# Kernel tuning notes

Measured on AMD Instinct MI355X. Metric: run time of the kernel, lower is better.

The kernel has to match this reference:

```python
import jax, jax.numpy as jnp
import numpy as np

N_NODES = 15000
N_EDGES = 400000
H_DIM = 128
N_RELS = 237
N_BASES = 100


def rel_graph_conv(x, src, dst, etype, norm, V, comp, loop_w, bias, n_nodes):
    """DGL RelGraphConv with basis regularizer, self_loop=True, bias=True.

    W_r = sum_b comp[r, b] * V[b]; message m_e = (x[src_e] @ W_{etype_e}) * norm_e;
    h[v] = sum_{e: dst_e = v} m_e + x[v] @ loop_w + bias.
    Reordered as sum over bases to avoid materializing per-edge weights:
      h = sum_b segment_sum(coef[etype, b] * norm * x[src], dst) @ V[b]
    """
    x_src = x[src] * norm                      # [E, D] (norm is [E, 1])
    coef = comp[etype]                         # [E, B]
    d_out = V.shape[2]

    def body(acc, cv):
        c, Vb = cv                             # c: [E], Vb: [D, Dout]
        agg = jax.ops.segment_sum(x_src * c[:, None], dst, num_segments=n_nodes)
        return acc + agg @ Vb, None

    init = jnp.zeros((n_nodes, d_out), x.dtype)
    h, _ = jax.lax.scan(body, init, (coef.T, V))  # scan over B bases
    return h + bias + x @ loop_w


def setup_inputs() -> dict:
    key = jax.random.key(0)
    ks = jax.random.split(key, 16)
    s = 1.0 / np.sqrt(H_DIM)
    inp = {
        "nids": jnp.arange(N_NODES, dtype=jnp.int32),
        "src": jax.random.randint(ks[0], (N_EDGES,), 0, N_NODES),
        "dst": jax.random.randint(ks[1], (N_EDGES,), 0, N_NODES),
        "etype": jax.random.randint(ks[2], (N_EDGES,), 0, N_RELS),
        "norm": jax.random.uniform(ks[3], (N_EDGES, 1), dtype=jnp.float32),
        "edge_weights": jax.random.normal(ks[4], (N_EDGES,), dtype=jnp.float32),
        "emb": jax.random.normal(ks[5], (N_NODES, H_DIM), dtype=jnp.float32) * s,
        "V1": jax.random.normal(ks[6], (N_BASES, H_DIM, H_DIM), dtype=jnp.float32) * s,
        "comp1": jax.random.normal(ks[7], (N_RELS, N_BASES), dtype=jnp.float32) * (1.0 / np.sqrt(N_BASES)),
        "loop1": jax.random.normal(ks[8], (H_DIM, H_DIM), dtype=jnp.float32) * s,
        "bias1": jnp.zeros((H_DIM,), dtype=jnp.float32),
        "V2": jax.random.normal(ks[9], (N_BASES, H_DIM, H_DIM), dtype=jnp.float32) * s,
        "comp2": jax.random.normal(ks[10], (N_RELS, N_BASES), dtype=jnp.float32) * (1.0 / np.sqrt(N_BASES)),
        "loop2": jax.random.normal(ks[11], (H_DIM, H_DIM), dtype=jnp.float32) * s,
        "bias2": jnp.zeros((H_DIM,), dtype=jnp.float32),
    }
    return inp


def reference(nids, src, dst, etype, norm, edge_weights, emb, V1, comp1, loop1, bias1, V2, comp2, loop2, bias2):
    # edge_weights is accepted but unused by the original forward.
    x = emb[nids]                                              # embedding lookup
    n = x.shape[0]
    h = jax.nn.relu(rel_graph_conv(x, src, dst, etype, norm, V1, comp1, loop1, bias1, n))
    # dropout(p=0.2) treated as identity (eval mode)
    h = rel_graph_conv(h, src, dst, etype, norm, V2, comp2, loop2, bias2, n)
    return h
```

## Files before the change

### kernel.cpp

```cpp
#include <hip/hip_runtime.h>
#include <hip/hip_bf16.h>


typedef unsigned short u16;
typedef unsigned int   u32;
typedef __bf16 bf16x8 __attribute__((ext_vector_type(8)));
typedef float  f32x4  __attribute__((ext_vector_type(4)));
typedef u32    u32x2  __attribute__((ext_vector_type(2)));

#define N_NODES 15000
#define N_EDGES 400000
#define N_RELS  237
#define N_BASES 100
#define NT_MAX  1800
#define NB_SORT 196
#define CHUNK   2048

__device__ __forceinline__ u32 packbf(float a, float b) {
    u16 lo = __builtin_bit_cast(u16, (__bf16)a);
    u16 hi = __builtin_bit_cast(u16, (__bf16)b);
    return (u32)lo | ((u32)hi << 16);
}
__device__ __forceinline__ float bfbits2f(u32 hi16) {
    u32 x = hi16 << 16;
    return __builtin_bit_cast(float, x);
}

__global__ __launch_bounds__(256) void histA_kernel(const int* __restrict__ etype,
                                                    int* __restrict__ blockHist) {
    __shared__ int hh[256];
    int tid = threadIdx.x, b = blockIdx.x;
    hh[tid] = 0;
    __syncthreads();
    int e0 = b * CHUNK;
    int e1 = e0 + CHUNK; if (e1 > N_EDGES) e1 = N_EDGES;
    for (int e = e0 + tid; e < e1; e += 256)
        atomicAdd(&hh[etype[e]], 1);
    __syncthreads();
    if (tid < N_RELS) blockHist[tid * NB_SORT + b] = hh[tid];
}

__global__ __launch_bounds__(256) void scanB_kernel(const int* __restrict__ blockHist,
                                                    int* __restrict__ baseOff,
                                                    int2* __restrict__ tiles,
                                                    int* __restrict__ tileCount) {
    __shared__ int h[256], o[256], to[256];
    int tid = threadIdx.x;
    int sum = 0;
    if (tid < N_RELS)
        for (int b = 0; b < NB_SORT; ++b) sum += blockHist[tid * NB_SORT + b];
    h[tid] = (tid < N_RELS) ? sum : 0;
    __syncthreads();
    if (tid == 0) {
        int run = 0, tc = 0;
        for (int r = 0; r < N_RELS; ++r) {
            o[r] = run; run += h[r];
            to[r] = tc; tc += (h[r] + 255) >> 8;
        }
        *tileCount = tc;
    }
    __syncthreads();
    if (tid < N_RELS) {
        int n = h[tid], t0 = to[tid], base = o[tid];
        for (int t = 0; t * 256 < n; ++t) {
            int nE = n - t * 256; if (nE > 256) nE = 256;
            tiles[t0 + t] = make_int2(base + t * 256, (tid << 9) | nE);
        }
        int run = base;
        for (int b = 0; b < NB_SORT; ++b) {
            baseOff[tid * NB_SORT + b] = run;
            run += blockHist[tid * NB_SORT + b];
        }
    }
}

__global__ __launch_bounds__(256) void scatterC_kernel(const int* __restrict__ etype,
                                                       const int* __restrict__ src,
                                                       const float* __restrict__ norm,
                                                       const int* __restrict__ baseOff,
                                                       int* __restrict__ perm,
                                                       int* __restrict__ srcPerm,
                                                       float* __restrict__ normPerm) {
    __shared__ int lcur[256];
    int tid = threadIdx.x, b = blockIdx.x;
    if (tid < N_RELS) lcur[tid] = baseOff[tid * NB_SORT + b];
    __syncthreads();
    int e0 = b * CHUNK;
    int e1 = e0 + CHUNK; if (e1 > N_EDGES) e1 = N_EDGES;
    for (int e = e0 + tid; e < e1; e += 256) {
        int r = etype[e];
        int pos = atomicAdd(&lcur[r], 1);
        perm[pos] = e;
        srcPerm[pos] = src[e];
        normPerm[pos] = norm[e];
    }
}

__global__ __launch_bounds__(256) void zeroDeg_kernel(int* __restrict__ deg) {
    int i = blockIdx.x * 256 + threadIdx.x;
    if (i < N_NODES) deg[i] = 0;
}
__global__ __launch_bounds__(256) void degcnt_kernel(const int* __restrict__ dst,
                                                     int* __restrict__ deg) {
    for (int e = blockIdx.x * 256 + threadIdx.x; e < N_EDGES; e += gridDim.x * 256)
        atomicAdd(&deg[dst[e]], 1);
}
__global__ __launch_bounds__(256) void scanDeg_kernel(const int* __restrict__ deg,
                                                      int* __restrict__ rowptr,
                                                      int* __restrict__ cursor) {
    __shared__ int part[256];
    int tid = threadIdx.x;
    const int R = 59;
    int lo = tid * R, hi = lo + R; if (hi > N_NODES + 1) hi = N_NODES + 1;
    int s = 0;
    for (int i = lo; i < hi; ++i) s += (i < N_NODES) ? deg[i] : 0;
    part[tid] = s;
    __syncthreads();
    if (tid == 0) {
        int run = 0;
        for (int t = 0; t < 256; ++t) { int tmp = part[t]; part[t] = run; run += tmp; }
    }
    __syncthreads();
    int run = part[tid];
    for (int i = lo; i < hi; ++i) {
        rowptr[i] = run; cursor[i] = run;
        run += (i < N_NODES) ? deg[i] : 0;
    }
}
__global__ __launch_bounds__(256) void scatterDst_kernel(const int* __restrict__ dst,
                                                         const int* __restrict__ perm,
                                                         int* __restrict__ cursor,
                                                         int* __restrict__ dstSlots) {
    for (int s = blockIdx.x * 256 + threadIdx.x; s < N_EDGES; s += gridDim.x * 256) {
        int e = perm[s];
        int v = dst[e];
        int pos = atomicAdd(&cursor[v], 1);
        dstSlots[pos] = s;
    }
}

__global__ __launch_bounds__(256) void wgemm_kernel(const float* __restrict__ comp,
                                                    const float* __restrict__ V,
                                                    u16* __restrict__ outRM) {
    __shared__ float cls[128 * 33];
    __shared__ float vls[32 * 256];
    int tid = threadIdx.x;
    int r0 = blockIdx.x * 32, n0 = blockIdx.y * 256;
    for (int idx = tid; idx < 32 * 128; idx += 256) {
        int rr = idx >> 7, b = idx & 127;
        float v = 0.f;
        if (b < N_BASES && (r0 + rr) < N_RELS) v = comp[(size_t)(r0 + rr) * N_BASES + b];
        cls[b * 33 + rr] = v;
    }
    float acc[4][8];
    #pragma unroll
    for (int i = 0; i < 4; ++i)
        #pragma unroll
        for (int j = 0; j < 8; ++j) acc[i][j] = 0.f;
    int rgrp = tid >> 5, ngrp = tid & 31;
    for (int bc = 0; bc < 4; ++bc) {
        __syncthreads();
        for (int idx = tid; idx < 32 * 256; idx += 256) {
            int bb = idx >> 8, n = idx & 255;
            int b = bc * 32 + bb;
            vls[idx] = (b < N_BASES) ? V[(size_t)b * 16384 + n0 + n] : 0.f;
        }
        __syncthreads();
        #pragma unroll 4
        for (int bb = 0; bb < 32; ++bb) {
            float a_[4];
            #pragma unroll
            for (int i = 0; i < 4; ++i) a_[i] = cls[(bc * 32 + bb) * 33 + rgrp * 4 + i];
            float4 b0 = *(const float4*)&vls[bb * 256 + ngrp * 8];
            float4 b1 = *(const float4*)&vls[bb * 256 + ngrp * 8 + 4];
            #pragma unroll
            for (int i = 0; i < 4; ++i) {
                acc[i][0] += a_[i] * b0.x; acc[i][1] += a_[i] * b0.y;
                acc[i][2] += a_[i] * b0.z; acc[i][3] += a_[i] * b0.w;
                acc[i][4] += a_[i] * b1.x; acc[i][5] += a_[i] * b1.y;
                acc[i][6] += a_[i] * b1.z; acc[i][7] += a_[i] * b1.w;
            }
        }
    }
    #pragma unroll
    for (int i = 0; i < 4; ++i) {
        int r = r0 + rgrp * 4 + i;
        if (r < N_RELS) {
            bf16x8 pk;
            #pragma unroll
            for (int j = 0; j < 8; ++j) pk[j] = (__bf16)acc[i][j];
            *(bf16x8*)(outRM + (size_t)r * 16384 + n0 + ngrp * 8) = pk;
        }
    }
}

__global__ __launch_bounds__(256) void transp_kernel(const u16* __restrict__ in,
                                                     u16* __restrict__ outT) {
    __shared__ u16 tls[128 * 130];
    int r = blockIdx.x, tid = threadIdx.x;
    const u32* inu = (const u32*)(in + (size_t)r * 16384);
    #pragma unroll
    for (int i = 0; i < 32; ++i) {
        int idx = i * 256 + tid;
        u32 v = inu[idx];
        int k = idx >> 6, jp = idx & 63;
        tls[k * 130 + jp * 2]     = (u16)(v & 0xffffu);
        tls[k * 130 + jp * 2 + 1] = (u16)(v >> 16);
    }
    __syncthreads();
    u32* outu = (u32*)(outT + (size_t)r * 16384);
    #pragma unroll
    for (int i = 0; i < 32; ++i) {
        int idx = i * 256 + tid;
        int col = idx >> 6, kk2 = idx & 63;
        u32 v = (u32)tls[(2 * kk2) * 130 + col] | ((u32)tls[(2 * kk2 + 1) * 130 + col] << 16);
        outu[col * 64 + kk2] = v;
    }
}

__global__ __launch_bounds__(256) void loopT_kernel(const float* __restrict__ lw,
                                                    u16* __restrict__ outT) {
    int tid = threadIdx.x;
    u32* outu = (u32*)outT;
    #pragma unroll
    for (int i = 0; i < 32; ++i) {
        int idx = i * 256 + tid;
        int col = idx >> 6, kk2 = idx & 63;
        float a = lw[(size_t)(2 * kk2) * 128 + col];
        float b = lw[(size_t)(2 * kk2 + 1) * 128 + col];
        outu[col * 64 + kk2] = packbf(a, b);
    }
}

__global__ __launch_bounds__(256) void xbf_kernel(const float* __restrict__ x,
                                                  u16* __restrict__ xbf,
                                                  int reluIn) {
    int i = blockIdx.x * 256 + threadIdx.x;
    if (i >= N_NODES * 16) return;
    const float4* xp = (const float4*)x;
    float4 f0 = xp[i * 2], f1 = xp[i * 2 + 1];
    if (reluIn) {
        f0.x = fmaxf(f0.x, 0.f); f0.y = fmaxf(f0.y, 0.f);
        f0.z = fmaxf(f0.z, 0.f); f0.w = fmaxf(f0.w, 0.f);
        f1.x = fmaxf(f1.x, 0.f); f1.y = fmaxf(f1.y, 0.f);
        f1.z = fmaxf(f1.z, 0.f); f1.w = fmaxf(f1.w, 0.f);
    }
    uint4 pk;
    pk.x = packbf(f0.x, f0.y); pk.y = packbf(f0.z, f0.w);
    pk.z = packbf(f1.x, f1.y); pk.w = packbf(f1.z, f1.w);
    ((uint4*)xbf)[i] = pk;
}

__global__ __launch_bounds__(256) void init_mfma_kernel(const float* __restrict__ xin,
                                                        const u16* __restrict__ lwT,
                                                        const float* __restrict__ bias,
                                                        float* __restrict__ hout,
                                                        int reluIn) {
    __shared__ u16 xlds[8192];
    int v0 = blockIdx.x * 64;
    int tid = threadIdx.x, lane = tid & 63, w = tid >> 6;

    bf16x8 bfr[2][4];
    #pragma unroll
    for (int n2 = 0; n2 < 2; ++n2) {
        int col = w * 32 + n2 * 16 + (lane & 15);
        #pragma unroll
        for (int ks = 0; ks < 4; ++ks) {
            int k0 = ks * 32 + (lane >> 4) * 8;
            bfr[n2][ks] = *(const bf16x8*)(lwT + (size_t)col * 128 + k0);
        }
    }

    {
        int s = tid >> 2, p = tid & 3;
        int row = v0 + s;
        if (row < N_NODES) {
            const float4* xr = (const float4*)(xin + (size_t)row * 128 + p * 32);
            #pragma unroll
            for (int c = 0; c < 4; ++c) {
                float4 f0 = xr[c * 2], f1 = xr[c * 2 + 1];
                if (reluIn) {
                    f0.x = fmaxf(f0.x, 0.f); f0.y = fmaxf(f0.y, 0.f);
                    f0.z = fmaxf(f0.z, 0.f); f0.w = fmaxf(f0.w, 0.f);
                    f1.x = fmaxf(f1.x, 0.f); f1.y = fmaxf(f1.y, 0.f);
                    f1.z = fmaxf(f1.z, 0.f); f1.w = fmaxf(f1.w, 0.f);
                }
                bf16x8 pk;
                pk[0] = (__bf16)f0.x; pk[1] = (__bf16)f0.y;
                pk[2] = (__bf16)f0.z; pk[3] = (__bf16)f0.w;
                pk[4] = (__bf16)f1.x; pk[5] = (__bf16)f1.y;
                pk[6] = (__bf16)f1.z; pk[7] = (__bf16)f1.w;
                int ch = p * 4 + c;
                *(bf16x8*)((char*)xlds + s * 256 + ((ch * 16) ^ ((s & 7) << 4))) = pk;
            }
        } else {
            bf16x8 z = {(__bf16)0.f, (__bf16)0.f, (__bf16)0.f, (__bf16)0.f,
                        (__bf16)0.f, (__bf16)0.f, (__bf16)0.f, (__bf16)0.f};
            #pragma unroll
            for (int c = 0; c < 4; ++c) {
                int ch = p * 4 + c;
                *(bf16x8*)((char*)xlds + s * 256 + ((ch * 16) ^ ((s & 7) << 4))) = z;
            }
        }
    }
    __syncthreads();

    #pragma unroll
    for (int rt = 0; rt < 4; ++rt) {
        bf16x8 af[4];
        int arow = rt * 16 + (lane & 15);
        #pragma unroll
        for (int ks = 0; ks < 4; ++ks) {
            int k0 = ks * 32 + (lane >> 4) * 8;
            af[ks] = *(const bf16x8*)((const char*)xlds + arow * 256 + ((k0 * 2) ^ ((arow & 7) << 4)));
        }
        f32x4 acc[2];
        acc[0] = (f32x4){0.f, 0.f, 0.f, 0.f};
        acc[1] = (f32x4){0.f, 0.f, 0.f, 0.f};
        #pragma unroll
        for (int ks = 0; ks < 4; ++ks) {
            acc[0] = __builtin_amdgcn_mfma_f32_16x16x32_bf16(bfr[0][ks], af[ks], acc[0], 0, 0, 0);
            acc[1] = __builtin_amdgcn_mfma_f32_16x16x32_bf16(bfr[1][ks], af[ks], acc[1], 0, 0, 0);
        }
        int orow = v0 + rt * 16 + (lane & 15);
        if (orow < N_NODES) {
            #pragma unroll
            for (int n2 = 0; n2 < 2; ++n2) {
                int fbase = w * 32 + n2 * 16 + ((lane >> 4) << 2);
                float4 bv = *(const float4*)(bias + fbase);
                float4 o;
                o.x = acc[n2][0] + bv.x; o.y = acc[n2][1] + bv.y;
                o.z = acc[n2][2] + bv.z; o.w = acc[n2][3] + bv.w;
                *(float4*)(hout + (size_t)orow * 128 + fbase) = o;
            }
        }
    }
}

__global__ __launch_bounds__(256) void msg_kernel(const u16* __restrict__ xbf,
                                                  const int* __restrict__ srcPerm,
                                                  const int2* __restrict__ tiles,
                                                  const int* __restrict__ tileCount,
                                                  const u16* __restrict__ WbtT,
                                                  u16* __restrict__ msg) {
    __shared__ u16 xlds[8192];
    int bid = blockIdx.x;
    int tile = (bid & 7) * (NT_MAX / 8) + (bid >> 3);
    if (tile >= *tileCount) return;
    int2 td = tiles[tile];
    int slot0 = td.x;
    int r  = td.y >> 9;
    int nE = td.y & 511;
    int tid = threadIdx.x, lane = tid & 63, w = tid >> 6;

    bf16x8 bfr[2][4];
    #pragma unroll
    for (int n2 = 0; n2 < 2; ++n2) {
        int col = w * 32 + n2 * 16 + (lane & 15);
        #pragma unroll
        for (int ks = 0; ks < 4; ++ks) {
            int k0 = ks * 32 + (lane >> 4) * 8;
            bfr[n2][ks] = *(const bf16x8*)(WbtT + (size_t)r * 16384 + col * 128 + k0);
        }
    }

    for (int s0 = 0; s0 < nE; s0 += 64) {
        int cnt = nE - s0; if (cnt > 64) cnt = 64;
        __syncthreads();
        {
            int s = tid >> 2, p = tid & 3;
            if (s < cnt) {
                int xrow = srcPerm[slot0 + s0 + s];
                const uint4* xr = (const uint4*)(xbf + (size_t)xrow * 128);
                #pragma unroll
                for (int c = 0; c < 4; ++c) {
                    int ch = p * 4 + c;
                    *(uint4*)((char*)xlds + s * 256 + ((ch * 16) ^ ((s & 7) << 4))) = xr[ch];
                }
            } else {
                uint4 z = {0u, 0u, 0u, 0u};
                #pragma unroll
                for (int c = 0; c < 4; ++c) {
                    int ch = p * 4 + c;
                    *(uint4*)((char*)xlds + s * 256 + ((ch * 16) ^ ((s & 7) << 4))) = z;
                }
            }
        }
        __syncthreads();

        #pragma unroll
        for (int rt = 0; rt < 4; ++rt) {
            bf16x8 af[4];
            int arow = rt * 16 + (lane & 15);
            #pragma unroll
            for (int ks = 0; ks < 4; ++ks) {
                int k0 = ks * 32 + (lane >> 4) * 8;
                af[ks] = *(const bf16x8*)((const char*)xlds + arow * 256 + ((k0 * 2) ^ ((arow & 7) << 4)));
            }
            f32x4 acc[2];
            acc[0] = (f32x4){0.f, 0.f, 0.f, 0.f};
            acc[1] = (f32x4){0.f, 0.f, 0.f, 0.f};
            #pragma unroll
            for (int ks = 0; ks < 4; ++ks) {
                acc[0] = __builtin_amdgcn_mfma_f32_16x16x32_bf16(bfr[0][ks], af[ks], acc[0], 0, 0, 0);
                acc[1] = __builtin_amdgcn_mfma_f32_16x16x32_bf16(bfr[1][ks], af[ks], acc[1], 0, 0, 0);
            }
            int srow = rt * 16 + (lane & 15);
            if (srow < cnt) {
                int slot = slot0 + s0 + srow;
                #pragma unroll
                for (int n2 = 0; n2 < 2; ++n2) {
                    int fbase = w * 32 + n2 * 16 + ((lane >> 4) << 2);
                    u32x2 pk;
                    pk.x = packbf(acc[n2][0], acc[n2][1]);
                    pk.y = packbf(acc[n2][2], acc[n2][3]);
                    *(u32x2*)(msg + (size_t)slot * 128 + fbase) = pk;
                }
            }
        }
    }
}

__global__ __launch_bounds__(256) void reduce_kernel(const u32* __restrict__ msg32,
                                                     const float* __restrict__ normPerm,
                                                     const int* __restrict__ rowptr,
                                                     const int* __restrict__ dstSlots,
                                                     float* __restrict__ h) {
    int v = blockIdx.x * 4 + (threadIdx.x >> 6);
    int lane = threadIdx.x & 63;
    if (v >= N_NODES) return;
    int p0 = rowptr[v], p1 = rowptr[v + 1];
    float a0 = 0.f, a1 = 0.f, b0 = 0.f, b1 = 0.f;
    int j = p0;
    for (; j + 3 < p1; j += 4) {
        int s0 = dstSlots[j], s1 = dstSlots[j + 1];
        int s2 = dstSlots[j + 2], s3 = dstSlots[j + 3];
        float n0 = normPerm[s0], n1 = normPerm[s1];
        float n2 = normPerm[s2], n3 = normPerm[s3];
        u32 m0 = __builtin_nontemporal_load(msg32 + (size_t)s0 * 64 + lane);
        u32 m1 = __builtin_nontemporal_load(msg32 + (size_t)s1 * 64 + lane);
        u32 m2 = __builtin_nontemporal_load(msg32 + (size_t)s2 * 64 + lane);
        u32 m3 = __builtin_nontemporal_load(msg32 + (size_t)s3 * 64 + lane);
        a0 += n0 * bfbits2f(m0 & 0xffffu); a1 += n0 * bfbits2f(m0 >> 16);
        b0 += n1 * bfbits2f(m1 & 0xffffu); b1 += n1 * bfbits2f(m1 >> 16);
        a0 += n2 * bfbits2f(m2 & 0xffffu); a1 += n2 * bfbits2f(m2 >> 16);
        b0 += n3 * bfbits2f(m3 & 0xffffu); b1 += n3 * bfbits2f(m3 >> 16);
    }
    for (; j < p1; ++j) {
        int s0 = dstSlots[j];
        float n0 = normPerm[s0];
        u32 m0 = __builtin_nontemporal_load(msg32 + (size_t)s0 * 64 + lane);
        a0 += n0 * bfbits2f(m0 & 0xffffu); a1 += n0 * bfbits2f(m0 >> 16);
    }
    float2 hv = *(float2*)(h + (size_t)v * 128 + lane * 2);
    hv.x += a0 + b0;
    hv.y += a1 + b1;
    *(float2*)(h + (size_t)v * 128 + lane * 2) = hv;
}

__global__ __launch_bounds__(256) void edge_atomic_kernel(const float* __restrict__ x,
                                                          const int* __restrict__ src,
                                                          const int* __restrict__ dst,
                                                          const float* __restrict__ norm,
                                                          const int* __restrict__ perm,
                                                          const int2* __restrict__ tiles,
                                                          const int* __restrict__ tileCount,
                                                          const u16* __restrict__ WbtT,
                                                          float* __restrict__ hout,
                                                          int reluIn) {
    __shared__ u16 xlds[8192];
    __shared__ int dlds[64];
    int bid = blockIdx.x;
    if (bid >= *tileCount) return;
    int2 td = tiles[bid];
    int slot0 = td.x;
    int r  = td.y >> 9;
    int nE = td.y & 511;
    int tid = threadIdx.x, lane = tid & 63, w = tid >> 6;

    bf16x8 bfr[2][4];
    #pragma unroll
    for (int n2 = 0; n2 < 2; ++n2) {
        int col = w * 32 + n2 * 16 + (lane & 15);
        #pragma unroll
        for (int ks = 0; ks < 4; ++ks) {
            int k0 = ks * 32 + (lane >> 4) * 8;
            bfr[n2][ks] = *(const bf16x8*)(WbtT + (size_t)r * 16384 + col * 128 + k0);
        }
    }

    for (int s0 = 0; s0 < nE; s0 += 64) {
        int cnt = nE - s0; if (cnt > 64) cnt = 64;
        __syncthreads();
        {
            int s = tid >> 2, p = tid & 3;
            if (s < cnt) {
                int e = perm[slot0 + s0 + s];
                int xrow = src[e];
                float nm = norm[e];
                if (p == 0) dlds[s] = dst[e];
                const float4* xr = (const float4*)(x + (size_t)xrow * 128 + p * 32);
                #pragma unroll
                for (int c = 0; c < 4; ++c) {
                    float4 f0 = xr[c * 2], f1 = xr[c * 2 + 1];
                    if (reluIn) {
                        f0.x = fmaxf(f0.x, 0.f); f0.y = fmaxf(f0.y, 0.f);
                        f0.z = fmaxf(f0.z, 0.f); f0.w = fmaxf(f0.w, 0.f);
                        f1.x = fmaxf(f1.x, 0.f); f1.y = fmaxf(f1.y, 0.f);
                        f1.z = fmaxf(f1.z, 0.f); f1.w = fmaxf(f1.w, 0.f);
                    }
                    bf16x8 pk;
                    pk[0] = (__bf16)(f0.x * nm); pk[1] = (__bf16)(f0.y * nm);
                    pk[2] = (__bf16)(f0.z * nm); pk[3] = (__bf16)(f0.w * nm);
                    pk[4] = (__bf16)(f1.x * nm); pk[5] = (__bf16)(f1.y * nm);
                    pk[6] = (__bf16)(f1.z * nm); pk[7] = (__bf16)(f1.w * nm);
                    int ch = p * 4 + c;
                    *(bf16x8*)((char*)xlds + s * 256 + ((ch * 16) ^ ((s & 7) << 4))) = pk;
                }
            } else {
                bf16x8 z = {(__bf16)0.f, (__bf16)0.f, (__bf16)0.f, (__bf16)0.f,
                            (__bf16)0.f, (__bf16)0.f, (__bf16)0.f, (__bf16)0.f};
                #pragma unroll
                for (int c = 0; c < 4; ++c) {
                    int ch = p * 4 + c;
                    *(bf16x8*)((char*)xlds + s * 256 + ((ch * 16) ^ ((s & 7) << 4))) = z;
                }
            }
        }
        __syncthreads();

        #pragma unroll
        for (int rt = 0; rt < 4; ++rt) {
            bf16x8 af[4];
            int arow = rt * 16 + (lane & 15);
            #pragma unroll
            for (int ks = 0; ks < 4; ++ks) {
                int k0 = ks * 32 + (lane >> 4) * 8;
                af[ks] = *(const bf16x8*)((const char*)xlds + arow * 256 + ((k0 * 2) ^ ((arow & 7) << 4)));
            }
            f32x4 acc[2];
            acc[0] = (f32x4){0.f, 0.f, 0.f, 0.f};
            acc[1] = (f32x4){0.f, 0.f, 0.f, 0.f};
            #pragma unroll
            for (int ks = 0; ks < 4; ++ks) {
                acc[0] = __builtin_amdgcn_mfma_f32_16x16x32_bf16(bfr[0][ks], af[ks], acc[0], 0, 0, 0);
                acc[1] = __builtin_amdgcn_mfma_f32_16x16x32_bf16(bfr[1][ks], af[ks], acc[1], 0, 0, 0);
            }
            int srow = rt * 16 + (lane & 15);
            if (srow < cnt) {
                int d = dlds[srow];
                #pragma unroll
                for (int n2 = 0; n2 < 2; ++n2) {
                    float* hp = hout + (size_t)d * 128 + w * 32 + n2 * 16 + ((lane >> 4) << 2);
                    #pragma unroll
                    for (int reg = 0; reg < 4; ++reg) atomicAdd(hp + reg, acc[n2][reg]);
                }
            }
        }
    }
}

extern "C" void kernel_launch(void* const* d_in, const int* in_sizes, int n_in,
                              void* d_out, int out_size, void* d_ws, size_t ws_size,
                              hipStream_t stream) {
    const int*   src   = (const int*)  d_in[1];
    const int*   dst   = (const int*)  d_in[2];
    const int*   etype = (const int*)  d_in[3];
    const float* norm  = (const float*)d_in[4];
    const float* emb   = (const float*)d_in[6];
    const float* V1    = (const float*)d_in[7];
    const float* comp1 = (const float*)d_in[8];
    const float* loop1 = (const float*)d_in[9];
    const float* bias1 = (const float*)d_in[10];
    const float* V2    = (const float*)d_in[11];
    const float* comp2 = (const float*)d_in[12];
    const float* loop2 = (const float*)d_in[13];
    const float* bias2 = (const float*)d_in[14];
    float* out = (float*)d_out;

    char* ws = (char*)d_ws;
    size_t off = 0;
    auto carve = [&](size_t bytes) -> void* {
        void* p = ws + off;
        off += (bytes + 255) & ~(size_t)255;
        return p;
    };
    const size_t WB = (size_t)N_RELS * 16384 * 2;
    u16* Wbt1      = (u16*)carve(WB);
    u16* Wbt2      = (u16*)carve(WB);
    void* uni      = carve(WB);
    u16*   rm      = (u16*)uni;
    float* h1      = (float*)uni;
    int*  perm     = (int*)carve((size_t)N_EDGES * 4);
    int*  srcPerm  = (int*)carve((size_t)N_EDGES * 4);
    float* normPerm= (float*)carve((size_t)N_EDGES * 4);
    int*  blockHist= (int*)carve((size_t)N_RELS * NB_SORT * 4);
    int*  baseOff  = (int*)carve((size_t)N_RELS * NB_SORT * 4);
    int2* tiles    = (int2*)carve((size_t)NT_MAX * 8);
    int*  tileCnt  = (int*)carve(256);
    u16*  lwT1     = (u16*)carve(128 * 128 * 2);
    u16*  lwT2     = (u16*)carve(128 * 128 * 2);
    int*  deg      = (int*)carve((size_t)N_NODES * 4);
    int*  rowptr   = (int*)carve((size_t)(N_NODES + 1) * 4);
    int*  cursor   = (int*)carve((size_t)(N_NODES + 1) * 4);
    int*  dstSlots = (int*)carve((size_t)N_EDGES * 4);
    u16*  xbf      = (u16*)carve((size_t)N_NODES * 128 * 2);
    u16*  msg      = (u16*)carve((size_t)N_EDGES * 128 * 2);
    bool twoPhase = (off <= ws_size);

    histA_kernel<<<NB_SORT, 256, 0, stream>>>(etype, blockHist);
    scanB_kernel<<<1, 256, 0, stream>>>(blockHist, baseOff, tiles, tileCnt);
    scatterC_kernel<<<NB_SORT, 256, 0, stream>>>(etype, src, norm, baseOff,
                                                 perm, srcPerm, normPerm);

    if (twoPhase) {
        zeroDeg_kernel<<<59, 256, 0, stream>>>(deg);
        degcnt_kernel<<<391, 256, 0, stream>>>(dst, deg);
        scanDeg_kernel<<<1, 256, 0, stream>>>(deg, rowptr, cursor);
        scatterDst_kernel<<<391, 256, 0, stream>>>(dst, perm, cursor, dstSlots);
    }

    dim3 wg(8, 64);
    wgemm_kernel<<<wg, 256, 0, stream>>>(comp1, V1, rm);
    transp_kernel<<<N_RELS, 256, 0, stream>>>(rm, Wbt1);
    wgemm_kernel<<<wg, 256, 0, stream>>>(comp2, V2, rm);
    transp_kernel<<<N_RELS, 256, 0, stream>>>(rm, Wbt2);
    loopT_kernel<<<1, 256, 0, stream>>>(loop1, lwT1);
    loopT_kernel<<<1, 256, 0, stream>>>(loop2, lwT2);

    if (twoPhase) {
        xbf_kernel<<<938, 256, 0, stream>>>(emb, xbf, 0);
        init_mfma_kernel<<<235, 256, 0, stream>>>(emb, lwT1, bias1, h1, 0);
        msg_kernel<<<NT_MAX, 256, 0, stream>>>(xbf, srcPerm, tiles, tileCnt,
                                               Wbt1, msg);
        reduce_kernel<<<3750, 256, 0, stream>>>((const u32*)msg, normPerm,
                                                rowptr, dstSlots, h1);
        xbf_kernel<<<938, 256, 0, stream>>>(h1, xbf, 1);
        init_mfma_kernel<<<235, 256, 0, stream>>>(h1, lwT2, bias2, out, 1);
        msg_kernel<<<NT_MAX, 256, 0, stream>>>(xbf, srcPerm, tiles, tileCnt,
                                               Wbt2, msg);
        reduce_kernel<<<3750, 256, 0, stream>>>((const u32*)msg, normPerm,
                                                rowptr, dstSlots, out);
    } else {
        init_mfma_kernel<<<235, 256, 0, stream>>>(emb, lwT1, bias1, h1, 0);
        edge_atomic_kernel<<<NT_MAX, 256, 0, stream>>>(emb, src, dst, norm, perm, tiles,
                                                       tileCnt, Wbt1, h1, 0);
        init_mfma_kernel<<<235, 256, 0, stream>>>(h1, lwT2, bias2, out, 1);
        edge_atomic_kernel<<<NT_MAX, 256, 0, stream>>>(h1, src, dst, norm, perm, tiles,
                                                       tileCnt, Wbt2, out, 1);
    }
}
```

Before: 486.0 us.

## Compute per-relation weights with MFMA bf16 GEMM writing transposed output directly

Replaces the FP32 scalar basis-combination GEMM and its separate transpose pass with a bf16 MFMA GEMM. V is pre-transposed and cast into a bf16 image and comp is cast to bf16, so the GEMM writes the transposed per-relation weight layout directly. This removes the row-major intermediate and the transpose kernel, and moves the 237x100x16384 combination onto matrix cores. The cost is extra small cast and transpose kernels, and the comp/V inputs are now rounded to bf16 before accumulation, which lowers precision slightly.

```diff
diff --git a/kernel.cpp b/kernel.cpp
--- a/kernel.cpp
+++ b/kernel.cpp
@@ -20,6 +20,9 @@
     u16 lo = __builtin_bit_cast(u16, (__bf16)a);
     u16 hi = __builtin_bit_cast(u16, (__bf16)b);
     return (u32)lo | ((u32)hi << 16);
+}
+__device__ __forceinline__ u16 bf16bits(float a) {
+    return __builtin_bit_cast(u16, (__bf16)a);
 }
 __device__ __forceinline__ float bfbits2f(u32 hi16) {
     u32 x = hi16 << 16;
@@ -139,82 +142,91 @@
     }
 }
 
-__global__ __launch_bounds__(256) void wgemm_kernel(const float* __restrict__ comp,
-                                                    const float* __restrict__ V,
-                                                    u16* __restrict__ outRM) {
-    __shared__ float cls[128 * 33];
-    __shared__ float vls[32 * 256];
-    int tid = threadIdx.x;
-    int r0 = blockIdx.x * 32, n0 = blockIdx.y * 256;
-    for (int idx = tid; idx < 32 * 128; idx += 256) {
-        int rr = idx >> 7, b = idx & 127;
-        float v = 0.f;
-        if (b < N_BASES && (r0 + rr) < N_RELS) v = comp[(size_t)(r0 + rr) * N_BASES + b];
-        cls[b * 33 + rr] = v;
-    }
-    float acc[4][8];
-    #pragma unroll
-    for (int i = 0; i < 4; ++i)
-        #pragma unroll
-        for (int j = 0; j < 8; ++j) acc[i][j] = 0.f;
-    int rgrp = tid >> 5, ngrp = tid & 31;
-    for (int bc = 0; bc < 4; ++bc) {
-        __syncthreads();
-        for (int idx = tid; idx < 32 * 256; idx += 256) {
-            int bb = idx >> 8, n = idx & 255;
-            int b = bc * 32 + bb;
-            vls[idx] = (b < N_BASES) ? V[(size_t)b * 16384 + n0 + n] : 0.f;
-        }
-        __syncthreads();
-        #pragma unroll 4
-        for (int bb = 0; bb < 32; ++bb) {
-            float a_[4];
-            #pragma unroll
-            for (int i = 0; i < 4; ++i) a_[i] = cls[(bc * 32 + bb) * 33 + rgrp * 4 + i];
-            float4 b0 = *(const float4*)&vls[bb * 256 + ngrp * 8];
-            float4 b1 = *(const float4*)&vls[bb * 256 + ngrp * 8 + 4];
-            #pragma unroll
-            for (int i = 0; i < 4; ++i) {
-                acc[i][0] += a_[i] * b0.x; acc[i][1] += a_[i] * b0.y;
-                acc[i][2] += a_[i] * b0.z; acc[i][3] += a_[i] * b0.w;
-                acc[i][4] += a_[i] * b1.x; acc[i][5] += a_[i] * b1.y;
-                acc[i][6] += a_[i] * b1.z; acc[i][7] += a_[i] * b1.w;
-            }
-        }
-    }
-    #pragma unroll
-    for (int i = 0; i < 4; ++i) {
-        int r = r0 + rgrp * 4 + i;
+__global__ __launch_bounds__(256) void compcast_kernel(const float* __restrict__ comp,
+                                                       u16* __restrict__ compbf) {
+    int idx = blockIdx.x * 256 + threadIdx.x;
+    if (idx >= 256 * 128) return;
+    int r = idx >> 7, b = idx & 127;
+    float v = (r < N_RELS && b < N_BASES) ? comp[(size_t)r * N_BASES + b] : 0.f;
+    compbf[idx] = bf16bits(v);
+}
+
+__global__ __launch_bounds__(256) void vt_kernel(const float* __restrict__ V,
+                                                 u16* __restrict__ aimg) {
+    __shared__ u16 t[128 * 130];
+    int k = blockIdx.x, tid = threadIdx.x;
+    #pragma unroll
+    for (int i = 0; i < 64; ++i) {
+        int idx = i * 256 + tid;
+        int b = idx >> 7, col = idx & 127;
+        float v = (b < N_BASES) ? V[(size_t)b * 16384 + k * 128 + col] : 0.f;
+        t[col * 130 + b] = bf16bits(v);
+    }
+    __syncthreads();
+    #pragma unroll
+    for (int i = 0; i < 64; ++i) {
+        int idx = i * 256 + tid;
+        int col = idx >> 7, b = idx & 127;
+        aimg[((size_t)col * 128 + k) * 128 + b] = t[col * 130 + b];
+    }
+}
+
+__global__ __launch_bounds__(256) void wgemmT_kernel(const u16* __restrict__ compbf,
+                                                     const u16* __restrict__ aimg,
+                                                     u16* __restrict__ Wbt) {
+    __shared__ u16 clds[8192];
+    int m0 = blockIdx.x * 64, n0 = blockIdx.y * 128;
+    int tid = threadIdx.x, lane = tid & 63, w = tid >> 6;
+
+    bf16x8 afr[2][4];
+    #pragma unroll
+    for (int n2 = 0; n2 < 2; ++n2) {
+        int j = n0 + w * 32 + n2 * 16 + (lane & 15);
+        #pragma unroll
+        for (int ks = 0; ks < 4; ++ks) {
+            int b0 = ks * 32 + (lane >> 4) * 8;
+            afr[n2][ks] = *(const bf16x8*)(aimg + (size_t)j * 128 + b0);
+        }
+    }
+    {
+        int s = tid >> 2, p = tid & 3;
+        const uint4* cr = (const uint4*)(compbf + (size_t)(m0 + s) * 128);
+        #pragma unroll
+        for (int c = 0; c < 4; ++c) {
+            int ch = p * 4 + c;
+            *(uint4*)((char*)clds + s * 256 + ((ch * 16) ^ ((s & 7) << 4))) = cr[ch];
+        }
+    }
+    __syncthreads();
+
+    #pragma unroll
+    for (int rt = 0; rt < 4; ++rt) {
+        bf16x8 cf[4];
+        int arow = rt * 16 + (lane & 15);
+        #pragma unroll
+        for (int ks = 0; ks < 4; ++ks) {
+            int k0 = ks * 32 + (lane >> 4) * 8;
+            cf[ks] = *(const bf16x8*)((const char*)clds + arow * 256 + ((k0 * 2) ^ ((arow & 7) << 4)));
+        }
+        f32x4 acc[2];
+        acc[0] = (f32x4){0.f, 0.f, 0.f, 0.f};
+        acc[1] = (f32x4){0.f, 0.f, 0.f, 0.f};
+        #pragma unroll
+        for (int ks = 0; ks < 4; ++ks) {
+            acc[0] = __builtin_amdgcn_mfma_f32_16x16x32_bf16(afr[0][ks], cf[ks], acc[0], 0, 0, 0);
+            acc[1] = __builtin_amdgcn_mfma_f32_16x16x32_bf16(afr[1][ks], cf[ks], acc[1], 0, 0, 0);
+        }
+        int r = m0 + rt * 16 + (lane & 15);
         if (r < N_RELS) {
-            bf16x8 pk;
-            #pragma unroll
-            for (int j = 0; j < 8; ++j) pk[j] = (__bf16)acc[i][j];
-            *(bf16x8*)(outRM + (size_t)r * 16384 + n0 + ngrp * 8) = pk;
-        }
-    }
-}
-
-__global__ __launch_bounds__(256) void transp_kernel(const u16* __restrict__ in,
-                                                     u16* __restrict__ outT) {
-    __shared__ u16 tls[128 * 130];
-    int r = blockIdx.x, tid = threadIdx.x;
-    const u32* inu = (const u32*)(in + (size_t)r * 16384);
-    #pragma unroll
-    for (int i = 0; i < 32; ++i) {
-        int idx = i * 256 + tid;
-        u32 v = inu[idx];
-        int k = idx >> 6, jp = idx & 63;
-        tls[k * 130 + jp * 2]     = (u16)(v & 0xffffu);
-        tls[k * 130 + jp * 2 + 1] = (u16)(v >> 16);
-    }
-    __syncthreads();
-    u32* outu = (u32*)(outT + (size_t)r * 16384);
-    #pragma unroll
-    for (int i = 0; i < 32; ++i) {
-        int idx = i * 256 + tid;
-        int col = idx >> 6, kk2 = idx & 63;
-        u32 v = (u32)tls[(2 * kk2) * 130 + col] | ((u32)tls[(2 * kk2 + 1) * 130 + col] << 16);
-        outu[col * 64 + kk2] = v;
+            #pragma unroll
+            for (int n2 = 0; n2 < 2; ++n2) {
+                int jb = n0 + w * 32 + n2 * 16 + ((lane >> 4) << 2);
+                u32x2 pk;
+                pk.x = packbf(acc[n2][0], acc[n2][1]);
+                pk.y = packbf(acc[n2][2], acc[n2][3]);
+                *(u32x2*)(Wbt + (size_t)r * 16384 + jb) = pk;
+            }
+        }
     }
 }
 
@@ -588,9 +600,7 @@
     const size_t WB = (size_t)N_RELS * 16384 * 2;
     u16* Wbt1      = (u16*)carve(WB);
     u16* Wbt2      = (u16*)carve(WB);
-    void* uni      = carve(WB);
-    u16*   rm      = (u16*)uni;
-    float* h1      = (float*)uni;
+    float* h1      = (float*)carve((size_t)N_NODES * 128 * 4);
     int*  perm     = (int*)carve((size_t)N_EDGES * 4);
     int*  srcPerm  = (int*)carve((size_t)N_EDGES * 4);
     float* normPerm= (float*)carve((size_t)N_EDGES * 4);
@@ -600,6 +610,9 @@
     int*  tileCnt  = (int*)carve(256);
     u16*  lwT1     = (u16*)carve(128 * 128 * 2);
     u16*  lwT2     = (u16*)carve(128 * 128 * 2);
+    u16*  compbf1  = (u16*)carve(256 * 128 * 2);
+    u16*  compbf2  = (u16*)carve(256 * 128 * 2);
+    u16*  aimg     = (u16*)carve((size_t)16384 * 128 * 2);
     int*  deg      = (int*)carve((size_t)N_NODES * 4);
     int*  rowptr   = (int*)carve((size_t)(N_NODES + 1) * 4);
     int*  cursor   = (int*)carve((size_t)(N_NODES + 1) * 4);
@@ -620,11 +633,13 @@
         scatterDst_kernel<<<391, 256, 0, stream>>>(dst, perm, cursor, dstSlots);
     }
 
-    dim3 wg(8, 64);
-    wgemm_kernel<<<wg, 256, 0, stream>>>(comp1, V1, rm);
-    transp_kernel<<<N_RELS, 256, 0, stream>>>(rm, Wbt1);
-    wgemm_kernel<<<wg, 256, 0, stream>>>(comp2, V2, rm);
-    transp_kernel<<<N_RELS, 256, 0, stream>>>(rm, Wbt2);
+    dim3 wgg(4, 128);
+    compcast_kernel<<<128, 256, 0, stream>>>(comp1, compbf1);
+    compcast_kernel<<<128, 256, 0, stream>>>(comp2, compbf2);
+    vt_kernel<<<128, 256, 0, stream>>>(V1, aimg);
+    wgemmT_kernel<<<wgg, 256, 0, stream>>>(compbf1, aimg, Wbt1);
+    vt_kernel<<<128, 256, 0, stream>>>(V2, aimg);
+    wgemmT_kernel<<<wgg, 256, 0, stream>>>(compbf2, aimg, Wbt2);
     loopT_kernel<<<1, 256, 0, stream>>>(loop1, lwT1);
     loopT_kernel<<<1, 256, 0, stream>>>(loop2, lwT2);
 
```

Result: faster. 413.5 us (-14.9%).
